# Performance work log

Measured on AMD Instinct MI355X. Metric: run time of the kernel, lower is better.

## Reference

```python
import jax, jax.numpy as jnp
import numpy as np

BS = 8            # block_size
NFA = 0.35        # nfa_threshold
EPS = 1e-08


def setup_inputs() -> dict:
    key = jax.random.key(0)
    k1, k2 = jax.random.split(key)
    B, C, H, W = 16, 3, 512, 512
    ref = jax.random.uniform(k1, (B, C, H, W), dtype=jnp.float32)
    tgt = jax.random.uniform(k2, (B, C, H, W), dtype=jnp.float32)
    return {"ref": ref, "tgt": tgt}


def _luminance(x):
    w = jnp.array([0.299, 0.587, 0.114], dtype=x.dtype).reshape(1, 3, 1, 1)
    return (x * w).sum(axis=1, keepdims=True)  # (B,1,H,W)


def _cross_diffs(img):
    lum = _luminance(img) if img.shape[1] == 3 else img
    e_h = jnp.abs(lum[:, :, :, :-1] - lum[:, :, :, 1:])  # (B,1,H,W-1)
    e_v = jnp.abs(lum[:, :, :-1, :] - lum[:, :, 1:, :])  # (B,1,H-1,W)
    return lum, e_h, e_v


def _phase_mask(de_line_mean, n_lines, out_len, threshold):
    # de_line_mean: (B, n_lines) mean excess energy per line (col or row)
    # Returns (B, out_len) binary mask of boundary lines at winning phase.
    phase = jnp.arange(n_lines) % BS                       # (n_lines,)
    onehot = (phase[:, None] == jnp.arange(BS)[None, :]).astype(de_line_mean.dtype)  # (n_lines, BS)
    counts = onehot.sum(axis=0)                            # (BS,)
    sums = de_line_mean @ onehot                           # (B, BS)
    a_k = sums / counts
    total = de_line_mean.sum(axis=1, keepdims=True)        # (B,1)
    bg = (total - sums) / (n_lines - counts)
    ratio = a_k / (bg + EPS)                               # (B, BS)
    best_k = jnp.argmax(ratio, axis=1)                     # (B,)
    best_r = jnp.max(ratio, axis=1)                        # (B,)
    blocked = best_r > threshold                           # (B,)
    idx = jnp.arange(out_len)
    line_hit = (idx[None, :] % BS == best_k[:, None]) & (idx[None, :] < n_lines)
    return (line_hit & blocked[:, None]).astype(jnp.float32)  # (B, out_len)


def reference(ref, tgt):
    _, e_h_ref, e_v_ref = _cross_diffs(ref)
    lum_t, e_h_tgt, e_v_tgt = _cross_diffs(tgt)
    de_h = jnp.clip(e_h_tgt - e_h_ref, 0.0)  # (B,1,H,W-1)
    de_v = jnp.clip(e_v_tgt - e_v_ref, 0.0)  # (B,1,H-1,W)
    B, _, H, W = lum_t.shape
    threshold = 1.0 / NFA

    col_mean = de_h[:, 0].mean(axis=1)  # (B, W-1): mean over H per column
    row_mean = de_v[:, 0].mean(axis=2)  # (B, H-1): mean over W per row

    mask_h_cols = _phase_mask(col_mean, W - 1, W, threshold)  # (B, W)
    mask_v_rows = _phase_mask(row_mean, H - 1, H, threshold)  # (B, H)

    mask_h = jnp.broadcast_to(mask_h_cols[:, None, None, :], (B, 1, H, W))
    mask_v = jnp.broadcast_to(mask_v_rows[:, None, :, None], (B, 1, H, W))
    return ((mask_h + mask_v) > 0).astype(jnp.float32)
```

## Files before the change

### kernel.cpp

```cpp
#include <hip/hip_runtime.h>

#define BATCH 16
#define HH 512
#define WW 512
#define RSLICE 8
#define NSLICE (HH / RSLICE)

static constexpr size_t PLANE = (size_t)HH * WW;
static constexpr size_t COLP_ELEMS = (size_t)BATCH * NSLICE * WW;
static constexpr size_t ROWS_ELEMS = (size_t)BATCH * HH;

struct RowBuf {
  float2 r0, r1, r2, t0, t1, t2;
  float br0, br1, br2, bt0, bt1, bt2;
};

__device__ __forceinline__ void load_row(RowBuf& B, const float* __restrict__ rb,
                                         const float* __restrict__ tb, int row,
                                         int t, bool bnd) {
  const size_t o = (size_t)row * WW + 2 * t;
  B.r0 = *(const float2*)(rb + o);
  B.r1 = *(const float2*)(rb + o + PLANE);
  B.r2 = *(const float2*)(rb + o + 2 * PLANE);
  B.t0 = *(const float2*)(tb + o);
  B.t1 = *(const float2*)(tb + o + PLANE);
  B.t2 = *(const float2*)(tb + o + 2 * PLANE);
  if (bnd) {
    const size_t ob = o + 2;
    B.br0 = rb[ob]; B.br1 = rb[ob + PLANE]; B.br2 = rb[ob + 2 * PLANE];
    B.bt0 = tb[ob]; B.bt1 = tb[ob + PLANE]; B.bt2 = tb[ob + 2 * PLANE];
  }
}

__device__ __forceinline__ float lum3(float a, float b, float c) {
  return 0.299f * a + 0.587f * b + 0.114f * c;
}

__global__ __launch_bounds__(256) void jbd_reduce(const float* __restrict__ ref,
                                                  const float* __restrict__ tgt,
                                                  float* __restrict__ colp,
                                                  float* __restrict__ rows) {
  const int t = threadIdx.x;
  const int lane = t & 63;
  const int wid = t >> 6;
  const bool bnd = (lane == 63) && (t != 255);
  const int slice = blockIdx.x & (NSLICE - 1);
  const int b = blockIdx.x >> 6;
  const int r0 = slice * RSLICE;
  const float* rb = ref + (size_t)b * 3 * PLANE;
  const float* tb = tgt + (size_t)b * 3 * PLANE;
  __shared__ float rowpart[RSLICE][4];

  float ca0 = 0.f, ca1 = 0.f;
  float plr0 = 0.f, plr1 = 0.f, plt0 = 0.f, plt1 = 0.f;

  RowBuf X, Y;
  load_row(X, rb, tb, r0, t, bnd);
  load_row(Y, rb, tb, r0 + 1, t, bnd);

#pragma unroll
  for (int i = 0; i <= RSLICE; ++i) {
    RowBuf& C = (i & 1) ? Y : X;
    const float a0 = lum3(C.r0.x, C.r1.x, C.r2.x);
    const float a1 = lum3(C.r0.y, C.r1.y, C.r2.y);
    const float c0 = lum3(C.t0.x, C.t1.x, C.t2.x);
    const float c1 = lum3(C.t0.y, C.t1.y, C.t2.y);
    float blr = 0.f, blt = 0.f;
    if (bnd) {
      blr = lum3(C.br0, C.br1, C.br2);
      blt = lum3(C.bt0, C.bt1, C.bt2);
    }
    if (i + 2 <= RSLICE)
      load_row(C, rb, tb, min(r0 + i + 2, HH - 1), t, bnd);
    float nlr = __shfl_down(a0, 1);
    float nlt = __shfl_down(c0, 1);
    if (bnd) { nlr = blr; nlt = blt; }
    if (i < RSLICE) {
      ca0 += fmaxf(fabsf(c0 - c1) - fabsf(a0 - a1), 0.f);
      if (t < 255)
        ca1 += fmaxf(fabsf(c1 - nlt) - fabsf(a1 - nlr), 0.f);
    }
    if (i >= 1 && (r0 + i) < HH) {
      float dv = fmaxf(fabsf(c0 - plt0) - fabsf(a0 - plr0), 0.f)
               + fmaxf(fabsf(c1 - plt1) - fabsf(a1 - plr1), 0.f);
      dv += __shfl_xor(dv, 1);
      dv += __shfl_xor(dv, 2);
      dv += __shfl_xor(dv, 4);
      dv += __shfl_xor(dv, 8);
      dv += __shfl_xor(dv, 16);
      dv += __shfl_xor(dv, 32);
      if (lane == 0) rowpart[i - 1][wid] = dv;
    }
    plr0 = a0; plr1 = a1; plt0 = c0; plt1 = c1;
  }
  __syncthreads();
  if (t < RSLICE) {
    const int h = r0 + t;
    if (h < HH - 1)
      rows[(size_t)b * HH + h] =
          rowpart[t][0] + rowpart[t][1] + rowpart[t][2] + rowpart[t][3];
  }
  *(float2*)&colp[((size_t)b * NSLICE + slice) * WW + 2 * t] =
      make_float2(ca0, ca1);
}

__global__ __launch_bounds__(64) void jbd_phase(const float* __restrict__ colp,
                                                const float* __restrict__ rows,
                                                int* __restrict__ results) {
  const int dir = blockIdx.x & 1;
  const int b = blockIdx.x >> 1;
  const int t = threadIdx.x;
  float c0 = 0.f, c1 = 0.f, c2 = 0.f, c3 = 0.f;
  float c4 = 0.f, c5 = 0.f, c6 = 0.f, c7 = 0.f;
  if (dir == 0) {
#pragma unroll 4
    for (int sl = 0; sl < NSLICE; ++sl) {
      const float* p = colp + ((size_t)b * NSLICE + sl) * WW + 8 * t;
      const float4 u = *(const float4*)p;
      const float4 v = *(const float4*)(p + 4);
      c0 += u.x; c1 += u.y; c2 += u.z; c3 += u.w;
      c4 += v.x; c5 += v.y; c6 += v.z; c7 += v.w;
    }
  } else {
    const float* p = rows + (size_t)b * HH + 8 * t;
    const float4 u = *(const float4*)p;
    const float4 v = *(const float4*)(p + 4);
    c0 = u.x; c1 = u.y; c2 = u.z; c3 = u.w;
    c4 = v.x; c5 = v.y; c6 = v.z; c7 = v.w;
  }
  if (t == 63) c7 = 0.f;
  float ps[8] = {c0, c1, c2, c3, c4, c5, c6, c7};
  float tot = 0.f;
#pragma unroll
  for (int p = 0; p < 8; ++p) {
    float v = ps[p];
    v += __shfl_xor(v, 1);
    v += __shfl_xor(v, 2);
    v += __shfl_xor(v, 4);
    v += __shfl_xor(v, 8);
    v += __shfl_xor(v, 16);
    v += __shfl_xor(v, 32);
    v *= (1.0f / 512.0f);
    ps[p] = v;
    tot += v;
  }
  float best = -1.f;
  int bk = 0;
#pragma unroll
  for (int p = 0; p < 8; ++p) {
    const float cnt = (p == 7) ? 63.f : 64.f;
    const float a_k = ps[p] / cnt;
    const float bg = (tot - ps[p]) / (511.f - cnt);
    const float r = a_k / (bg + 1e-8f);
    if (r > best) { best = r; bk = p; }
  }
  if (t == 0) {
    results[4 * b + 2 * dir] = bk;
    results[4 * b + 2 * dir + 1] = (best > (float)(1.0 / 0.35)) ? 1 : 0;
  }
}

__global__ __launch_bounds__(256) void jbd_write(const int* __restrict__ results,
                                                 float* __restrict__ out) {
  const int idx = blockIdx.x * 256 + threadIdx.x;
  const int b = idx >> 16;
  const int rem = idx & 65535;
  const int h = rem >> 7;
  const int wq = rem & 127;
  const int4 rs = ((const int4*)results)[b];
  const bool rowm = (rs.w != 0) && ((h & 7) == rs.z) && (h < HH - 1);
  float4 o;
  float* po = (float*)&o;
  const int w0 = wq << 2;
#pragma unroll
  for (int j = 0; j < 4; ++j) {
    const int w = w0 + j;
    const bool colm = (rs.y != 0) && ((w & 7) == rs.x) && (w < WW - 1);
    po[j] = (rowm || colm) ? 1.0f : 0.0f;
  }
  ((float4*)out)[idx] = o;
}

extern "C" void kernel_launch(void* const* d_in, const int* in_sizes, int n_in,
                              void* d_out, int out_size, void* d_ws, size_t ws_size,
                              hipStream_t stream) {
  (void)in_sizes; (void)n_in; (void)out_size; (void)ws_size;
  const float* ref = (const float*)d_in[0];
  const float* tgt = (const float*)d_in[1];
  float* colp = (float*)d_ws;
  float* rows = colp + COLP_ELEMS;
  int* results = (int*)(rows + ROWS_ELEMS);
  jbd_reduce<<<BATCH * NSLICE, 256, 0, stream>>>(ref, tgt, colp, rows);
  jbd_phase<<<2 * BATCH, 64, 0, stream>>>(colp, rows, results);
  jbd_write<<<(BATCH * HH * WW / 4) / 256, 256, 0, stream>>>(results, (float*)d_out);
}
```

Before: 136.0 us.

## Stage per-slice luminance rows in shared memory with vectorized float4 loads

The reduce kernel now computes luminance for the 9 rows of its slice up front and stores it in shared memory. Half the threads handle ref and half handle tgt, each using float4 global loads. The compute loop then reads neighbours from shared memory, which replaces the register double-buffering, the boundary-lane extra loads and the shuffle-based right-neighbour exchange. This exposes more independent loads at once and simplifies the inner loop. In exchange it uses about 36 KB of LDS per block, which may limit occupancy, and it no longer overlaps loads with compute inside a block.

```diff
diff --git a/kernel.cpp b/kernel.cpp
--- a/kernel.cpp
+++ b/kernel.cpp
@@ -10,28 +10,6 @@
 static constexpr size_t COLP_ELEMS = (size_t)BATCH * NSLICE * WW;
 static constexpr size_t ROWS_ELEMS = (size_t)BATCH * HH;
 
-struct RowBuf {
-  float2 r0, r1, r2, t0, t1, t2;
-  float br0, br1, br2, bt0, bt1, bt2;
-};
-
-__device__ __forceinline__ void load_row(RowBuf& B, const float* __restrict__ rb,
-                                         const float* __restrict__ tb, int row,
-                                         int t, bool bnd) {
-  const size_t o = (size_t)row * WW + 2 * t;
-  B.r0 = *(const float2*)(rb + o);
-  B.r1 = *(const float2*)(rb + o + PLANE);
-  B.r2 = *(const float2*)(rb + o + 2 * PLANE);
-  B.t0 = *(const float2*)(tb + o);
-  B.t1 = *(const float2*)(tb + o + PLANE);
-  B.t2 = *(const float2*)(tb + o + 2 * PLANE);
-  if (bnd) {
-    const size_t ob = o + 2;
-    B.br0 = rb[ob]; B.br1 = rb[ob + PLANE]; B.br2 = rb[ob + 2 * PLANE];
-    B.bt0 = tb[ob]; B.bt1 = tb[ob + PLANE]; B.bt2 = tb[ob + 2 * PLANE];
-  }
-}
-
 __device__ __forceinline__ float lum3(float a, float b, float c) {
   return 0.299f * a + 0.587f * b + 0.114f * c;
 }
@@ -43,55 +21,61 @@
   const int t = threadIdx.x;
   const int lane = t & 63;
   const int wid = t >> 6;
-  const bool bnd = (lane == 63) && (t != 255);
   const int slice = blockIdx.x & (NSLICE - 1);
   const int b = blockIdx.x >> 6;
   const int r0 = slice * RSLICE;
-  const float* rb = ref + (size_t)b * 3 * PLANE;
-  const float* tb = tgt + (size_t)b * 3 * PLANE;
+  __shared__ float Lr[RSLICE + 1][WW];
+  __shared__ float Lt[RSLICE + 1][WW];
   __shared__ float rowpart[RSLICE][4];
 
+  {
+    const int g = t >> 7;
+    const int u = t & 127;
+    const float* base = (g ? tgt : ref) + (size_t)b * 3 * PLANE;
+    float* L = g ? &Lt[0][0] : &Lr[0][0];
+#pragma unroll
+    for (int k = 0; k <= RSLICE; ++k) {
+      const int row = min(r0 + k, HH - 1);
+      const size_t o = (size_t)row * WW + 4 * u;
+      const float4 p0 = *(const float4*)(base + o);
+      const float4 p1 = *(const float4*)(base + o + PLANE);
+      const float4 p2 = *(const float4*)(base + o + 2 * PLANE);
+      float4 l;
+      l.x = lum3(p0.x, p1.x, p2.x);
+      l.y = lum3(p0.y, p1.y, p2.y);
+      l.z = lum3(p0.z, p1.z, p2.z);
+      l.w = lum3(p0.w, p1.w, p2.w);
+      *(float4*)&L[k * WW + 4 * u] = l;
+    }
+  }
+  __syncthreads();
+
   float ca0 = 0.f, ca1 = 0.f;
-  float plr0 = 0.f, plr1 = 0.f, plt0 = 0.f, plt1 = 0.f;
-
-  RowBuf X, Y;
-  load_row(X, rb, tb, r0, t, bnd);
-  load_row(Y, rb, tb, r0 + 1, t, bnd);
-
+  const int c0i = 2 * t;
+  float lr0 = Lr[0][c0i], lr1 = Lr[0][c0i + 1];
+  float lt0 = Lt[0][c0i], lt1 = Lt[0][c0i + 1];
 #pragma unroll
-  for (int i = 0; i <= RSLICE; ++i) {
-    RowBuf& C = (i & 1) ? Y : X;
-    const float a0 = lum3(C.r0.x, C.r1.x, C.r2.x);
-    const float a1 = lum3(C.r0.y, C.r1.y, C.r2.y);
-    const float c0 = lum3(C.t0.x, C.t1.x, C.t2.x);
-    const float c1 = lum3(C.t0.y, C.t1.y, C.t2.y);
-    float blr = 0.f, blt = 0.f;
-    if (bnd) {
-      blr = lum3(C.br0, C.br1, C.br2);
-      blt = lum3(C.bt0, C.bt1, C.bt2);
+  for (int i = 0; i < RSLICE; ++i) {
+    const float nlr = Lr[i][c0i + 2];
+    const float nlt = Lt[i][c0i + 2];
+    ca0 += fmaxf(fabsf(lt0 - lt1) - fabsf(lr0 - lr1), 0.f);
+    if (t < 255)
+      ca1 += fmaxf(fabsf(lt1 - nlt) - fabsf(lr1 - nlr), 0.f);
+    const float xr0 = Lr[i + 1][c0i], xr1 = Lr[i + 1][c0i + 1];
+    const float xt0 = Lt[i + 1][c0i], xt1 = Lt[i + 1][c0i + 1];
+    float dv = 0.f;
+    if (r0 + i < HH - 1) {
+      dv = fmaxf(fabsf(xt0 - lt0) - fabsf(xr0 - lr0), 0.f)
+         + fmaxf(fabsf(xt1 - lt1) - fabsf(xr1 - lr1), 0.f);
     }
-    if (i + 2 <= RSLICE)
-      load_row(C, rb, tb, min(r0 + i + 2, HH - 1), t, bnd);
-    float nlr = __shfl_down(a0, 1);
-    float nlt = __shfl_down(c0, 1);
-    if (bnd) { nlr = blr; nlt = blt; }
-    if (i < RSLICE) {
-      ca0 += fmaxf(fabsf(c0 - c1) - fabsf(a0 - a1), 0.f);
-      if (t < 255)
-        ca1 += fmaxf(fabsf(c1 - nlt) - fabsf(a1 - nlr), 0.f);
-    }
-    if (i >= 1 && (r0 + i) < HH) {
-      float dv = fmaxf(fabsf(c0 - plt0) - fabsf(a0 - plr0), 0.f)
-               + fmaxf(fabsf(c1 - plt1) - fabsf(a1 - plr1), 0.f);
-      dv += __shfl_xor(dv, 1);
-      dv += __shfl_xor(dv, 2);
-      dv += __shfl_xor(dv, 4);
-      dv += __shfl_xor(dv, 8);
-      dv += __shfl_xor(dv, 16);
-      dv += __shfl_xor(dv, 32);
-      if (lane == 0) rowpart[i - 1][wid] = dv;
-    }
-    plr0 = a0; plr1 = a1; plt0 = c0; plt1 = c1;
+    dv += __shfl_xor(dv, 1);
+    dv += __shfl_xor(dv, 2);
+    dv += __shfl_xor(dv, 4);
+    dv += __shfl_xor(dv, 8);
+    dv += __shfl_xor(dv, 16);
+    dv += __shfl_xor(dv, 32);
+    if (lane == 0) rowpart[i][wid] = dv;
+    lr0 = xr0; lr1 = xr1; lt0 = xt0; lt1 = xt1;
   }
   __syncthreads();
   if (t < RSLICE) {
@@ -100,7 +84,7 @@
       rows[(size_t)b * HH + h] =
           rowpart[t][0] + rowpart[t][1] + rowpart[t][2] + rowpart[t][3];
   }
-  *(float2*)&colp[((size_t)b * NSLICE + slice) * WW + 2 * t] =
+  *(float2*)&colp[((size_t)b * NSLICE + slice) * WW + c0i] =
       make_float2(ca0, ca1);
 }
 
```

New measurement: 136.6 us. No clear change (+0.5%).
